# Kernel optimization log

Measured on AMD Instinct MI355X. Metric: run time of the kernel, lower is better.

## Reference

```python
import jax, jax.numpy as jnp
import numpy as np

DEPTH = 24
DLAT = 80      # latent_dim
H = 8          # latent_heads
DH = 64        # latent_dim_head
INNER = H * DH # 512
FFD = 2 * DLAT # FeedForward mult=2 -> 160
B = 64         # hardcoded in forward reshape
N = 128        # hardcoded max_num_nodes
MHD = 20       # multi_hop_max_dist
EF = 3         # edge feature count (meaned over by edge encoder)
EPS = 1e-5


def _ln(x, g, b):
    m = x.mean(-1, keepdims=True)
    v = ((x - m) ** 2).mean(-1, keepdims=True)
    return (x - m) / jnp.sqrt(v + EPS) * g + b


def setup_inputs() -> dict:
    key = jax.random.key(0)
    ks = jax.random.split(key, 24)
    std = 0.02 / np.sqrt(DEPTH)
    inp = {}
    # integer graph inputs
    inp['spatial_pos'] = jax.random.randint(ks[0], (B, N, N), 0, 40, dtype=jnp.int32)
    inp['edge_input'] = jax.random.randint(ks[1], (B, N, N, MHD, EF), 0, 64, dtype=jnp.int32)
    inp['x_nodes'] = jax.random.randint(ks[2], (B, N), 0, 64, dtype=jnp.int32)
    inp['indeg'] = jax.random.randint(ks[3], (B, N), 0, 64, dtype=jnp.int32)
    inp['outdeg'] = jax.random.randint(ks[4], (B, N), 0, 64, dtype=jnp.int32)
    # embedding tables (init_params: Embedding std=0.02)
    inp['atom_emb'] = 0.02 * jax.random.normal(ks[5], (64, DLAT), dtype=jnp.float32)
    inp['indeg_emb'] = 0.02 * jax.random.normal(ks[6], (64, DLAT), dtype=jnp.float32)
    inp['outdeg_emb'] = 0.02 * jax.random.normal(ks[7], (64, DLAT), dtype=jnp.float32)
    inp['edge_emb'] = 0.02 * jax.random.normal(ks[8], (64, 1), dtype=jnp.float32)
    inp['edge_dis_w'] = 0.02 * jax.random.normal(ks[9], (40,), dtype=jnp.float32)
    inp['spatial_emb'] = 0.02 * jax.random.normal(ks[10], (40, 1), dtype=jnp.float32)
    # per-layer stacked params (init_params: Linear std=0.02/sqrt(depth), bias 0)
    inp['ln1_g'] = jnp.ones((DEPTH, DLAT), jnp.float32)
    inp['ln1_b'] = jnp.zeros((DEPTH, DLAT), jnp.float32)
    inp['Wq'] = std * jax.random.normal(ks[11], (DEPTH, DLAT, INNER), dtype=jnp.float32)
    inp['Wkv'] = std * jax.random.normal(ks[12], (DEPTH, DLAT, 2 * INNER), dtype=jnp.float32)
    inp['Wo'] = std * jax.random.normal(ks[13], (DEPTH, INNER, DLAT), dtype=jnp.float32)
    inp['bo'] = jnp.zeros((DEPTH, DLAT), jnp.float32)
    inp['ln2_g'] = jnp.ones((DEPTH, DLAT), jnp.float32)
    inp['ln2_b'] = jnp.zeros((DEPTH, DLAT), jnp.float32)
    inp['W1'] = std * jax.random.normal(ks[14], (DEPTH, DLAT, FFD), dtype=jnp.float32)
    inp['b1'] = jnp.zeros((DEPTH, FFD), jnp.float32)
    inp['W2'] = std * jax.random.normal(ks[15], (DEPTH, FFD, DLAT), dtype=jnp.float32)
    inp['b2'] = jnp.zeros((DEPTH, DLAT), jnp.float32)
    # final head: LayerNorm + Linear(latent_dim, 1)
    inp['lnf_g'] = jnp.ones((DLAT,), jnp.float32)
    inp['lnf_b'] = jnp.zeros((DLAT,), jnp.float32)
    inp['Wf'] = std * jax.random.normal(ks[16], (DLAT, 1), dtype=jnp.float32)
    inp['bf'] = jnp.zeros((1,), jnp.float32)
    return inp


def reference(spatial_pos, edge_input, x_nodes, indeg, outdeg,
              atom_emb, indeg_emb, outdeg_emb, edge_emb, edge_dis_w, spatial_emb,
              ln1_g, ln1_b, Wq, Wkv, Wo, bo, ln2_g, ln2_b, W1, b1, W2, b2,
              lnf_g, lnf_b, Wf, bf):
    # --- graph structural bias ---
    sp_bias = spatial_emb[spatial_pos, 0]                       # [B,N,N]
    sp = jnp.where(spatial_pos == 0, 1, spatial_pos)
    sp = jnp.where(sp > 1, sp - 1, sp)
    sp = jnp.clip(sp, 0, MHD)
    e = edge_emb[edge_input, 0].mean(axis=-1)                   # [B,N,N,MHD] (mean over edge feats)
    e = (e * edge_dis_w[:MHD]).sum(-1) / sp.astype(jnp.float32) # per-hop scale, sum hops, normalize
    bias = e + sp_bias                                          # [B,N,N]
    # --- node embeddings ---
    x = atom_emb[x_nodes] + indeg_emb[indeg] + outdeg_emb[outdeg]  # [B,N,DLAT]
    scale = DH ** -0.5

    def layer(x, p):
        g1, be1, wq, wkv, wo, bo_, g2, be2, w1, bb1, w2, bb2 = p
        h = _ln(x, g1, be1)
        q = (h @ wq).reshape(B, N, H, DH)
        kv = h @ wkv
        k = kv[..., :INNER].reshape(B, N, H, DH)
        v = kv[..., INNER:].reshape(B, N, H, DH)
        sim = jnp.einsum('bihd,bjhd->bhij', q, k) * scale + bias[:, None]
        a = jax.nn.softmax(sim, axis=-1)
        o = jnp.einsum('bhij,bjhd->bihd', a, v).reshape(B, N, INNER)
        x = o @ wo + bo_ + x
        h = _ln(x, g2, be2)
        x = jax.nn.gelu(h @ w1 + bb1, approximate=False) @ w2 + bb2 + x
        return x, None

    x, _ = jax.lax.scan(layer, x, (ln1_g, ln1_b, Wq, Wkv, Wo, bo, ln2_g, ln2_b, W1, b1, W2, b2))
    pooled = x.mean(axis=1)                                     # Reduce 'b n d -> b d'
    return _ln(pooled, lnf_g, lnf_b) @ Wf + bf                  # [B,1]
```

## Files before the change

kernel.cpp:

```cpp
#include <hip/hip_runtime.h>
#include <math.h>

#define BDIM 64
#define NNODE 128
#define DLAT 80
#define NHEAD 8
#define DH 64
#define INNER 512
#define FFD 160
#define DEPTH 24
#define MROWS (BDIM * NNODE)

using bf16x8 = __attribute__((ext_vector_type(8))) short;
using f32x4  = __attribute__((ext_vector_type(4))) float;

#define MFMA(a, b, c) __builtin_amdgcn_mfma_f32_16x16x32_bf16((a), (b), (c), 0, 0, 0)

static __device__ __forceinline__ short f2bf(float f) {
    union { float f; unsigned u; } v; v.f = f;
    unsigned r = v.u + 0x7fffu + ((v.u >> 16) & 1u);
    return (short)(r >> 16);
}

__global__ __launch_bounds__(256) void wconv_kernel(
    const float* __restrict__ in, short* __restrict__ out, int K, int N, int Kp)
{
    __shared__ float t[64][65];
    int L = blockIdx.z;
    const float* src = in + (size_t)L * K * N;
    short* dst = out + (size_t)L * N * Kp;
    int n0 = blockIdx.x * 64, k0 = blockIdx.y * 64;
    int tx = threadIdx.x & 63, ty = threadIdx.x >> 6;
    for (int ki = ty; ki < 64; ki += 4) {
        int k = k0 + ki, n = n0 + tx;
        t[ki][tx] = (k < K && n < N) ? src[(size_t)k * N + n] : 0.f;
    }
    __syncthreads();
    for (int ni = ty; ni < 64; ni += 4) {
        int n = n0 + ni, k = k0 + tx;
        if (n < N && k < Kp) dst[(size_t)n * Kp + k] = f2bf(t[tx][ni]);
    }
}

__global__ __launch_bounds__(256) void bias_kernel(
    const int* __restrict__ spp, const int* __restrict__ ei,
    const float* __restrict__ edge_emb, const float* __restrict__ edw,
    const float* __restrict__ sp_emb, float* __restrict__ biasb)
{
    __shared__ float ee[64], ew[20], se[40];
    int tid = threadIdx.x;
    if (tid < 64) ee[tid] = edge_emb[tid];
    if (tid < 20) ew[tid] = edw[tid];
    if (tid < 40) se[tid] = sp_emb[tid];
    __syncthreads();

    int idx = blockIdx.x * 256 + tid;
    int spv = spp[idx];
    float spb = se[spv];
    int sp = min(20, max(1, spv - 1));

    const int4* p = (const int4*)(ei + (size_t)idx * 60);
    int e[60];
#pragma unroll
    for (int t = 0; t < 15; ++t) {
        int4 v = p[t];
        e[4*t+0] = v.x; e[4*t+1] = v.y; e[4*t+2] = v.z; e[4*t+3] = v.w;
    }
    float acc = 0.f;
#pragma unroll
    for (int m = 0; m < 20; ++m) {
        float s = ee[e[3*m]] + ee[e[3*m+1]] + ee[e[3*m+2]];
        acc += s * ew[m];
    }
    biasb[idx] = acc * (1.0f/3.0f) / (float)sp + spb;
}

__global__ __launch_bounds__(256) void node_emb_kernel(
    const int* __restrict__ xn, const int* __restrict__ ind, const int* __restrict__ outd,
    const float* __restrict__ ae, const float* __restrict__ ie, const float* __restrict__ oe,
    float* __restrict__ x)
{
    int idx = blockIdx.x * 256 + threadIdx.x;
    int e = idx / DLAT, d = idx % DLAT;
    x[idx] = ae[xn[e]*DLAT + d] + ie[ind[e]*DLAT + d] + oe[outd[e]*DLAT + d];
}

__global__ __launch_bounds__(256) void ln1_kernel(
    const float* __restrict__ x, const float* __restrict__ g,
    const float* __restrict__ be, short* __restrict__ lnx)
{
    int row = blockIdx.x * 128 + (threadIdx.x >> 1), sub = threadIdx.x & 1;
    const float* xr = x + (size_t)row * DLAT + sub * 40;
    float4 v[10];
#pragma unroll
    for (int i = 0; i < 10; ++i) v[i] = *(const float4*)(xr + i * 4);
    float s = 0.f;
#pragma unroll
    for (int i = 0; i < 10; ++i) s += v[i].x + v[i].y + v[i].z + v[i].w;
    s += __shfl_xor(s, 1);
    float mean = s * 0.0125f;
    float var = 0.f;
#pragma unroll
    for (int i = 0; i < 10; ++i) {
        float d;
        d = v[i].x - mean; var += d * d;
        d = v[i].y - mean; var += d * d;
        d = v[i].z - mean; var += d * d;
        d = v[i].w - mean; var += d * d;
    }
    var += __shfl_xor(var, 1);
    float rstd = 1.0f / sqrtf(var * 0.0125f + 1e-5f);
    short* dst = lnx + (size_t)row * 96 + sub * 40;
#pragma unroll
    for (int i = 0; i < 10; ++i) {
        int c = sub * 40 + i * 4;
        float4 g4 = *(const float4*)(g + c);
        float4 b4 = *(const float4*)(be + c);
        short4 o;
        o.x = f2bf((v[i].x - mean) * rstd * g4.x + b4.x);
        o.y = f2bf((v[i].y - mean) * rstd * g4.y + b4.y);
        o.z = f2bf((v[i].z - mean) * rstd * g4.z + b4.z);
        o.w = f2bf((v[i].w - mean) * rstd * g4.w + b4.w);
        *(short4*)(dst + i * 4) = o;
    }
    short4 z4; z4.x = z4.y = z4.z = z4.w = 0;
    *(short4*)(lnx + (size_t)row * 96 + 80 + sub * 8) = z4;
    *(short4*)(lnx + (size_t)row * 96 + 84 + sub * 8) = z4;
}

__global__ __launch_bounds__(512, 4) void attn2_kernel(
    const short* __restrict__ lnx, const float* __restrict__ biasb,
    const short* __restrict__ Wq_t, const short* __restrict__ Wkv_t,
    short* __restrict__ obuf)
{
    extern __shared__ short smem[];
    short* qh  = smem;
    short* kh  = smem + 9216;
    short* vth = smem + 18432;
    short* ph  = smem;
    short* ot  = smem + 18432;

    int tid = threadIdx.x;
    int lane = tid & 63, w = tid >> 6, l15 = lane & 15, lk = lane >> 4;
    int b = blockIdx.x >> 3, h = blockIdx.x & 7;

    float breg[8][4];
    {
        const float* bp = biasb + ((size_t)b * NNODE + w * 16) * NNODE;
#pragma unroll
        for (int jf = 0; jf < 8; ++jf)
#pragma unroll
            for (int r = 0; r < 4; ++r)
                breg[jf][r] = bp[(lk * 4 + r) * NNODE + jf * 16 + l15];
    }

    {
        const short* lb = lnx + (size_t)b * NNODE * 96;
        bf16x8 a[3];
#pragma unroll
        for (int ss = 0; ss < 3; ++ss)
            a[ss] = *(const bf16x8*)(lb + (w * 16 + l15) * 96 + ss * 32 + lk * 8);

        {
            f32x4 acc[4] = {};
#pragma unroll
            for (int ss = 0; ss < 3; ++ss)
#pragma unroll
                for (int nf = 0; nf < 4; ++nf) {
                    bf16x8 bv = *(const bf16x8*)(Wq_t + (size_t)(h * 64 + nf * 16 + l15) * 96 + ss * 32 + lk * 8);
                    acc[nf] = MFMA(a[ss], bv, acc[nf]);
                }
#pragma unroll
            for (int nf = 0; nf < 4; ++nf)
#pragma unroll
                for (int r = 0; r < 4; ++r)
                    qh[(w * 16 + lk * 4 + r) * 72 + nf * 16 + l15] = f2bf(acc[nf][r]);
        }
        {
            f32x4 acc[4] = {};
#pragma unroll
            for (int ss = 0; ss < 3; ++ss)
#pragma unroll
                for (int nf = 0; nf < 4; ++nf) {
                    bf16x8 bv = *(const bf16x8*)(Wkv_t + (size_t)(h * 64 + nf * 16 + l15) * 96 + ss * 32 + lk * 8);
                    acc[nf] = MFMA(a[ss], bv, acc[nf]);
                }
#pragma unroll
            for (int nf = 0; nf < 4; ++nf)
#pragma unroll
                for (int r = 0; r < 4; ++r)
                    kh[(w * 16 + lk * 4 + r) * 72 + nf * 16 + l15] = f2bf(acc[nf][r]);
        }
        {
            f32x4 acc[4] = {};
#pragma unroll
            for (int ss = 0; ss < 3; ++ss)
#pragma unroll
                for (int nf = 0; nf < 4; ++nf) {
                    bf16x8 bv = *(const bf16x8*)(Wkv_t + (size_t)(INNER + h * 64 + nf * 16 + l15) * 96 + ss * 32 + lk * 8);
                    acc[nf] = MFMA(a[ss], bv, acc[nf]);
                }
#pragma unroll
            for (int nf = 0; nf < 4; ++nf)
#pragma unroll
                for (int r = 0; r < 4; ++r)
                    vth[(nf * 16 + l15) * 136 + w * 16 + lk * 4 + r] = f2bf(acc[nf][r]);
        }
    }
    __syncthreads();

    f32x4 sc[8] = {};
#pragma unroll
    for (int ss = 0; ss < 2; ++ss) {
        bf16x8 qa = *(const bf16x8*)(qh + (w * 16 + l15) * 72 + ss * 32 + lk * 8);
#pragma unroll
        for (int jf = 0; jf < 8; ++jf) {
            bf16x8 bv = *(const bf16x8*)(kh + (jf * 16 + l15) * 72 + ss * 32 + lk * 8);
            sc[jf] = MFMA(qa, bv, sc[jf]);
        }
    }
    __syncthreads();

    float rinv[4];
#pragma unroll
    for (int r = 0; r < 4; ++r) {
        float sv[8];
#pragma unroll
        for (int jf = 0; jf < 8; ++jf) sv[jf] = sc[jf][r] * 0.125f + breg[jf][r];
        float mx = sv[0];
#pragma unroll
        for (int jf = 1; jf < 8; ++jf) mx = fmaxf(mx, sv[jf]);
        mx = fmaxf(mx, __shfl_xor(mx, 1));
        mx = fmaxf(mx, __shfl_xor(mx, 2));
        mx = fmaxf(mx, __shfl_xor(mx, 4));
        mx = fmaxf(mx, __shfl_xor(mx, 8));
        float e[8], sum = 0.f;
#pragma unroll
        for (int jf = 0; jf < 8; ++jf) { e[jf] = __expf(sv[jf] - mx); sum += e[jf]; }
        sum += __shfl_xor(sum, 1);
        sum += __shfl_xor(sum, 2);
        sum += __shfl_xor(sum, 4);
        sum += __shfl_xor(sum, 8);
        rinv[r] = 1.0f / sum;
        int row = w * 16 + lk * 4 + r;
#pragma unroll
        for (int jf = 0; jf < 8; ++jf)
            ph[row * 136 + jf * 16 + l15] = f2bf(e[jf]);
    }
    __syncthreads();

    f32x4 o[4] = {};
#pragma unroll
    for (int ks = 0; ks < 4; ++ks) {
        bf16x8 pa = *(const bf16x8*)(ph + (w * 16 + l15) * 136 + ks * 32 + lk * 8);
#pragma unroll
        for (int nf = 0; nf < 4; ++nf) {
            bf16x8 bv = *(const bf16x8*)(vth + (nf * 16 + l15) * 136 + ks * 32 + lk * 8);
            o[nf] = MFMA(pa, bv, o[nf]);
        }
    }
    __syncthreads();

#pragma unroll
    for (int nf = 0; nf < 4; ++nf)
#pragma unroll
        for (int r = 0; r < 4; ++r)
            ot[(w * 16 + lk * 4 + r) * 68 + nf * 16 + l15] = f2bf(o[nf][r] * rinv[r]);
    __syncthreads();

    {
        int row = tid >> 2, q4 = tid & 3;
        const short* src = ot + row * 68 + q4 * 16;
        short* dst = obuf + ((size_t)b * NNODE + row) * INNER + h * 64 + q4 * 16;
#pragma unroll
        for (int qq = 0; qq < 4; ++qq)
            *(uint2*)(dst + qq * 4) = *(const uint2*)(src + qq * 4);
    }
}

__global__ __launch_bounds__(512, 2) void tail2_kernel(
    const short* __restrict__ obuf, const float* __restrict__ xin,
    const short* __restrict__ Wo_t, const float* __restrict__ boL,
    const float* __restrict__ g2, const float* __restrict__ be2,
    const short* __restrict__ W1_t, const float* __restrict__ b1L,
    const short* __restrict__ W2_t, const float* __restrict__ b2L,
    float* __restrict__ xout,
    const float* __restrict__ g1n, const float* __restrict__ be1n,
    short* __restrict__ lnx)
{
    __shared__ float xmid[32 * 84];
    __shared__ short h2s[32 * 104];
    __shared__ short ffhs[32 * 168];

    int tid = threadIdx.x;
    int lane = tid & 63, w = tid >> 6, l15 = lane & 15, lk = lane >> 4;
    int b = blockIdx.x >> 2, qq = blockIdx.x & 3;
    int R0 = qq * 32;
    int wr = w >> 2, wn = w & 3;

    int n0_5 = (wn == 0) ? 0 : (wn + 1);
    int nc_5 = (wn == 0) ? 2 : 1;
    int n0_10 = (wn < 2) ? wn * 3 : 6 + (wn - 2) * 2;
    int nc_10 = (wn < 2) ? 3 : 2;

    {
        const short* og = obuf + ((size_t)b * NNODE + R0) * INNER;
        f32x4 acc[2] = {};
#pragma unroll 4
        for (int ks = 0; ks < 16; ++ks) {
            bf16x8 aa = *(const bf16x8*)(og + (wr * 16 + l15) * INNER + lk * 8 + ks * 32);
#pragma unroll
            for (int j = 0; j < 2; ++j)
                if (j < nc_5) {
                    bf16x8 bv = *(const bf16x8*)(Wo_t + (size_t)((n0_5 + j) * 16 + l15) * INNER + lk * 8 + ks * 32);
                    acc[j] = MFMA(aa, bv, acc[j]);
                }
        }
#pragma unroll
        for (int j = 0; j < 2; ++j)
            if (j < nc_5)
#pragma unroll
                for (int r = 0; r < 4; ++r) {
                    int row = wr * 16 + lk * 4 + r, col = (n0_5 + j) * 16 + l15;
                    xmid[row * 84 + col] = acc[j][r] + boL[col] +
                        xin[((size_t)b * NNODE + R0 + row) * DLAT + col];
                }
    }
    __syncthreads();

    {
        int row = tid >> 4, sub = tid & 15;
        float v[5];
#pragma unroll
        for (int e = 0; e < 5; ++e) v[e] = xmid[row * 84 + sub * 5 + e];
        float s = v[0] + v[1] + v[2] + v[3] + v[4];
        s += __shfl_xor(s, 1); s += __shfl_xor(s, 2);
        s += __shfl_xor(s, 4); s += __shfl_xor(s, 8);
        float mean = s * 0.0125f;
        float var = 0.f;
#pragma unroll
        for (int e = 0; e < 5; ++e) { float d = v[e] - mean; var += d * d; }
        var += __shfl_xor(var, 1); var += __shfl_xor(var, 2);
        var += __shfl_xor(var, 4); var += __shfl_xor(var, 8);
        float rstd = 1.0f / sqrtf(var * 0.0125f + 1e-5f);
#pragma unroll
        for (int e = 0; e < 5; ++e) {
            int c = sub * 5 + e;
            h2s[row * 104 + c] = f2bf((v[e] - mean) * rstd * g2[c] + be2[c]);
        }
        if (sub < 4) {
            short4 z4; z4.x = z4.y = z4.z = z4.w = 0;
            *(short4*)(h2s + row * 104 + 80 + sub * 4) = z4;
        }
    }
    __syncthreads();

    {
        f32x4 acc[3] = {};
#pragma unroll
        for (int ss = 0; ss < 3; ++ss) {
            bf16x8 aa = *(const bf16x8*)(h2s + (wr * 16 + l15) * 104 + lk * 8 + ss * 32);
#pragma unroll
            for (int j = 0; j < 3; ++j)
                if (j < nc_10) {
                    bf16x8 bv = *(const bf16x8*)(W1_t + (size_t)((n0_10 + j) * 16 + l15) * 96 + lk * 8 + ss * 32);
                    acc[j] = MFMA(aa, bv, acc[j]);
                }
        }
#pragma unroll
        for (int j = 0; j < 3; ++j)
            if (j < nc_10)
#pragma unroll
                for (int r = 0; r < 4; ++r) {
                    int row = wr * 16 + lk * 4 + r, c = (n0_10 + j) * 16 + l15;
                    float vv = acc[j][r] + b1L[c];
                    vv = 0.5f * vv * (1.0f + erff(vv * 0.70710678118654752f));
                    ffhs[row * 168 + c] = f2bf(vv);
                }
    }
    __syncthreads();

    {
        f32x4 acc[2] = {};
#pragma unroll
        for (int ks = 0; ks < 5; ++ks) {
            bf16x8 aa = *(const bf16x8*)(ffhs + (wr * 16 + l15) * 168 + lk * 8 + ks * 32);
#pragma unroll
            for (int j = 0; j < 2; ++j)
                if (j < nc_5) {
                    bf16x8 bv = *(const bf16x8*)(W2_t + (size_t)((n0_5 + j) * 16 + l15) * FFD + lk * 8 + ks * 32);
                    acc[j] = MFMA(aa, bv, acc[j]);
                }
        }
#pragma unroll
        for (int j = 0; j < 2; ++j)
            if (j < nc_5)
#pragma unroll
                for (int r = 0; r < 4; ++r) {
                    int row = wr * 16 + lk * 4 + r, col = (n0_5 + j) * 16 + l15;
                    float vv = acc[j][r] + b2L[col] + xmid[row * 84 + col];
                    xout[((size_t)b * NNODE + R0 + row) * DLAT + col] = vv;
                    xmid[row * 84 + col] = vv;
                }
    }
    __syncthreads();

    if (g1n) {
        int row = tid >> 4, sub = tid & 15;
        float v[5];
#pragma unroll
        for (int e = 0; e < 5; ++e) v[e] = xmid[row * 84 + sub * 5 + e];
        float s = v[0] + v[1] + v[2] + v[3] + v[4];
        s += __shfl_xor(s, 1); s += __shfl_xor(s, 2);
        s += __shfl_xor(s, 4); s += __shfl_xor(s, 8);
        float mean = s * 0.0125f;
        float var = 0.f;
#pragma unroll
        for (int e = 0; e < 5; ++e) { float d = v[e] - mean; var += d * d; }
        var += __shfl_xor(var, 1); var += __shfl_xor(var, 2);
        var += __shfl_xor(var, 4); var += __shfl_xor(var, 8);
        float rstd = 1.0f / sqrtf(var * 0.0125f + 1e-5f);
        short* lr = lnx + ((size_t)b * NNODE + R0 + row) * 96;
#pragma unroll
        for (int e = 0; e < 5; ++e) {
            int c = sub * 5 + e;
            lr[c] = f2bf((v[e] - mean) * rstd * g1n[c] + be1n[c]);
        }
        if (sub < 8) { lr[80 + sub * 2] = 0; lr[81 + sub * 2] = 0; }
    }
}

__global__ __launch_bounds__(128) void final_kernel(
    const float* __restrict__ x, const float* __restrict__ g, const float* __restrict__ bta,
    const float* __restrict__ Wf, const float* __restrict__ bf, float* __restrict__ out)
{
    int bb = blockIdx.x;
    int t = threadIdx.x;
    __shared__ float pd[DLAT];
    __shared__ float red[2];
    __shared__ float rbuf[128];

    if (t < DLAT) {
        float s = 0.f;
        for (int n = 0; n < NNODE; ++n) s += x[((size_t)bb * NNODE + n) * DLAT + t];
        pd[t] = s * (1.0f / NNODE);
    }
    __syncthreads();
    if (t == 0) {
        float m = 0.f;
        for (int k = 0; k < DLAT; ++k) m += pd[k];
        m /= DLAT;
        float v = 0.f;
        for (int k = 0; k < DLAT; ++k) { float d = pd[k] - m; v += d * d; }
        v /= DLAT;
        red[0] = m; red[1] = 1.0f / sqrtf(v + 1e-5f);
    }
    __syncthreads();
    float contrib = 0.f;
    if (t < DLAT)
        contrib = ((pd[t] - red[0]) * red[1] * g[t] + bta[t]) * Wf[t];
    rbuf[t] = contrib;
    __syncthreads();
    if (t == 0) {
        float s = 0.f;
        for (int k = 0; k < DLAT; ++k) s += rbuf[k];
        out[bb] = s + bf[0];
    }
}

extern "C" void kernel_launch(void* const* d_in, const int* in_sizes, int n_in,
                              void* d_out, int out_size, void* d_ws, size_t ws_size,
                              hipStream_t stream)
{
    const int*   spatial_pos = (const int*)  d_in[0];
    const int*   edge_input  = (const int*)  d_in[1];
    const int*   x_nodes     = (const int*)  d_in[2];
    const int*   indeg       = (const int*)  d_in[3];
    const int*   outdeg      = (const int*)  d_in[4];
    const float* atom_emb    = (const float*)d_in[5];
    const float* indeg_emb   = (const float*)d_in[6];
    const float* outdeg_emb  = (const float*)d_in[7];
    const float* edge_emb    = (const float*)d_in[8];
    const float* edge_dis_w  = (const float*)d_in[9];
    const float* spatial_emb = (const float*)d_in[10];
    const float* ln1_g = (const float*)d_in[11];
    const float* ln1_b = (const float*)d_in[12];
    const float* Wq    = (const float*)d_in[13];
    const float* Wkv   = (const float*)d_in[14];
    const float* Wo    = (const float*)d_in[15];
    const float* bo    = (const float*)d_in[16];
    const float* ln2_g = (const float*)d_in[17];
    const float* ln2_b = (const float*)d_in[18];
    const float* W1    = (const float*)d_in[19];
    const float* b1    = (const float*)d_in[20];
    const float* W2    = (const float*)d_in[21];
    const float* b2    = (const float*)d_in[22];
    const float* lnf_g = (const float*)d_in[23];
    const float* lnf_b = (const float*)d_in[24];
    const float* Wf    = (const float*)d_in[25];
    const float* bf    = (const float*)d_in[26];

    char* wsb = (char*)d_ws;
    float* biasb = (float*)(wsb + 0);
    float* x0    = (float*)(wsb + 4194304);
    float* x1    = (float*)(wsb + 6815744);
    short* obuf  = (short*)(wsb + 9437184);
    short* Wq_t  = (short*)(wsb + 17825792);
    short* Wkv_t = (short*)(wsb + 20185088);
    short* Wo_t  = (short*)(wsb + 24903680);
    short* W1_t  = (short*)(wsb + 26869760);
    short* W2_t  = (short*)(wsb + 27607040);
    short* lnx   = (short*)(wsb + 28221440);

    static const int ATTN_LDS = 54272;
    hipFuncSetAttribute((const void*)attn2_kernel,
                        hipFuncAttributeMaxDynamicSharedMemorySize, ATTN_LDS);

    wconv_kernel<<<dim3(8, 2, 24), 256, 0, stream>>>(Wq,  Wq_t,  80, 512, 96);
    wconv_kernel<<<dim3(16, 2, 24), 256, 0, stream>>>(Wkv, Wkv_t, 80, 1024, 96);
    wconv_kernel<<<dim3(2, 8, 24), 256, 0, stream>>>(Wo,  Wo_t,  512, 80, 512);
    wconv_kernel<<<dim3(3, 2, 24), 256, 0, stream>>>(W1,  W1_t,  80, 160, 96);
    wconv_kernel<<<dim3(2, 3, 24), 256, 0, stream>>>(W2,  W2_t,  160, 80, 160);

    bias_kernel<<<4096, 256, 0, stream>>>(spatial_pos, edge_input, edge_emb,
                                          edge_dis_w, spatial_emb, biasb);
    node_emb_kernel<<<2560, 256, 0, stream>>>(x_nodes, indeg, outdeg,
                                              atom_emb, indeg_emb, outdeg_emb, x0);
    ln1_kernel<<<64, 256, 0, stream>>>(x0, ln1_g, ln1_b, lnx);

    for (int L = 0; L < DEPTH; ++L) {
        const float* xin  = (L & 1) ? x1 : x0;
        float*       xout = (L & 1) ? x0 : x1;
        attn2_kernel<<<512, 512, ATTN_LDS, stream>>>(
            lnx, biasb,
            Wq_t + (size_t)L * 512 * 96, Wkv_t + (size_t)L * 1024 * 96,
            obuf);
        const float* g1n  = (L < DEPTH - 1) ? (ln1_g + (L + 1) * DLAT) : nullptr;
        const float* be1n = (L < DEPTH - 1) ? (ln1_b + (L + 1) * DLAT) : nullptr;
        tail2_kernel<<<256, 512, 0, stream>>>(
            obuf, xin,
            Wo_t + (size_t)L * 80 * 512, bo + L * DLAT,
            ln2_g + L * DLAT, ln2_b + L * DLAT,
            W1_t + (size_t)L * 160 * 96, b1 + L * FFD,
            W2_t + (size_t)L * 80 * 160, b2 + L * DLAT,
            xout, g1n, be1n, lnx);
    }

    final_kernel<<<BDIM, 128, 0, stream>>>(x0, lnf_g, lnf_b, Wf, bf, (float*)d_out);
}
```

Measured before the change: 1.529 ms.

## Fuse whole forward into one persistent kernel with per-graph atomic flag sync

Replaces about fifty kernel launches (weight conversion, bias, embedding, LN, and per-layer attention and tail) with a single persistent kernel of 256 blocks. Each block owns one graph and 32 rows, keeps the residual stream in LDS, and syncs with the other three blocks of its graph through atomic counters instead of kernel boundaries. This removes launch gaps and global round trips of x between layers. In exchange each block now processes two heads serially, occupancy is limited by larger LDS use, and all 256 blocks must be co-resident or the spin-waits will deadlock.

```diff
diff --git a/kernel.cpp b/kernel.cpp
--- a/kernel.cpp
+++ b/kernel.cpp
@@ -4,12 +4,9 @@
 #define BDIM 64
 #define NNODE 128
 #define DLAT 80
-#define NHEAD 8
-#define DH 64
 #define INNER 512
 #define FFD 160
 #define DEPTH 24
-#define MROWS (BDIM * NNODE)
 
 using bf16x8 = __attribute__((ext_vector_type(8))) short;
 using f32x4  = __attribute__((ext_vector_type(4))) float;
@@ -22,127 +19,179 @@
     return (short)(r >> 16);
 }
 
-__global__ __launch_bounds__(256) void wconv_kernel(
-    const float* __restrict__ in, short* __restrict__ out, int K, int N, int Kp)
+__device__ __forceinline__ void wait_cnt(int* p, int target) {
+    if (threadIdx.x == 0)
+        while (__hip_atomic_load(p, __ATOMIC_ACQUIRE, __HIP_MEMORY_SCOPE_AGENT) < target)
+            __builtin_amdgcn_s_sleep(2);
+    __syncthreads();
+}
+__device__ __forceinline__ void arrive(int* p) {
+    __syncthreads();
+    if (threadIdx.x == 0)
+        __hip_atomic_fetch_add(p, 1, __ATOMIC_RELEASE, __HIP_MEMORY_SCOPE_AGENT);
+}
+
+__device__ __forceinline__ void conv_tile(
+    const float* __restrict__ src, short* __restrict__ dst,
+    int K, int N, int Kp, int n0, int k0, float* tbuf)
 {
-    __shared__ float t[64][65];
-    int L = blockIdx.z;
-    const float* src = in + (size_t)L * K * N;
-    short* dst = out + (size_t)L * N * Kp;
-    int n0 = blockIdx.x * 64, k0 = blockIdx.y * 64;
     int tx = threadIdx.x & 63, ty = threadIdx.x >> 6;
-    for (int ki = ty; ki < 64; ki += 4) {
+    for (int ki = ty; ki < 64; ki += 8) {
         int k = k0 + ki, n = n0 + tx;
-        t[ki][tx] = (k < K && n < N) ? src[(size_t)k * N + n] : 0.f;
+        tbuf[ki * 65 + tx] = (k < K && n < N) ? src[(size_t)k * N + n] : 0.f;
     }
     __syncthreads();
-    for (int ni = ty; ni < 64; ni += 4) {
+    for (int ni = ty; ni < 64; ni += 8) {
         int n = n0 + ni, k = k0 + tx;
-        if (n < N && k < Kp) dst[(size_t)n * Kp + k] = f2bf(t[tx][ni]);
-    }
-}
-
-__global__ __launch_bounds__(256) void bias_kernel(
+        if (n < N && k < Kp) dst[(size_t)n * Kp + k] = f2bf(tbuf[tx * 65 + ni]);
+    }
+    __syncthreads();
+}
+
+__device__ __forceinline__ void ln_rows_to_lnx(
+    const float* xper, int row, int sub,
+    const float* __restrict__ g, const float* __restrict__ be,
+    short* __restrict__ lnxbase)
+{
+    float v[5];
+#pragma unroll
+    for (int e = 0; e < 5; ++e) v[e] = xper[row * 84 + sub * 5 + e];
+    float s = v[0] + v[1] + v[2] + v[3] + v[4];
+    s += __shfl_xor(s, 1); s += __shfl_xor(s, 2);
+    s += __shfl_xor(s, 4); s += __shfl_xor(s, 8);
+    float mean = s * 0.0125f;
+    float var = 0.f;
+#pragma unroll
+    for (int e = 0; e < 5; ++e) { float d = v[e] - mean; var += d * d; }
+    var += __shfl_xor(var, 1); var += __shfl_xor(var, 2);
+    var += __shfl_xor(var, 4); var += __shfl_xor(var, 8);
+    float rstd = 1.0f / sqrtf(var * 0.0125f + 1e-5f);
+    short* lr = lnxbase + row * 96;
+#pragma unroll
+    for (int e = 0; e < 5; ++e) {
+        int c = sub * 5 + e;
+        lr[c] = f2bf((v[e] - mean) * rstd * g[c] + be[c]);
+    }
+    if (sub < 8) { lr[80 + sub * 2] = 0; lr[81 + sub * 2] = 0; }
+}
+
+__global__ __launch_bounds__(512, 2) void persist_kernel(
     const int* __restrict__ spp, const int* __restrict__ ei,
-    const float* __restrict__ edge_emb, const float* __restrict__ edw,
-    const float* __restrict__ sp_emb, float* __restrict__ biasb)
-{
-    __shared__ float ee[64], ew[20], se[40];
-    int tid = threadIdx.x;
-    if (tid < 64) ee[tid] = edge_emb[tid];
-    if (tid < 20) ew[tid] = edw[tid];
-    if (tid < 40) se[tid] = sp_emb[tid];
-    __syncthreads();
-
-    int idx = blockIdx.x * 256 + tid;
-    int spv = spp[idx];
-    float spb = se[spv];
-    int sp = min(20, max(1, spv - 1));
-
-    const int4* p = (const int4*)(ei + (size_t)idx * 60);
-    int e[60];
-#pragma unroll
-    for (int t = 0; t < 15; ++t) {
-        int4 v = p[t];
-        e[4*t+0] = v.x; e[4*t+1] = v.y; e[4*t+2] = v.z; e[4*t+3] = v.w;
-    }
-    float acc = 0.f;
-#pragma unroll
-    for (int m = 0; m < 20; ++m) {
-        float s = ee[e[3*m]] + ee[e[3*m+1]] + ee[e[3*m+2]];
-        acc += s * ew[m];
-    }
-    biasb[idx] = acc * (1.0f/3.0f) / (float)sp + spb;
-}
-
-__global__ __launch_bounds__(256) void node_emb_kernel(
     const int* __restrict__ xn, const int* __restrict__ ind, const int* __restrict__ outd,
     const float* __restrict__ ae, const float* __restrict__ ie, const float* __restrict__ oe,
-    float* __restrict__ x)
+    const float* __restrict__ edge_emb, const float* __restrict__ edw,
+    const float* __restrict__ sp_emb,
+    const float* __restrict__ Wq, const float* __restrict__ Wkv,
+    const float* __restrict__ Wo, const float* __restrict__ W1, const float* __restrict__ W2,
+    const float* __restrict__ ln1_g, const float* __restrict__ ln1_b,
+    const float* __restrict__ bo,
+    const float* __restrict__ ln2_g, const float* __restrict__ ln2_b,
+    const float* __restrict__ b1, const float* __restrict__ b2,
+    const float* __restrict__ lnf_g, const float* __restrict__ lnf_b,
+    const float* __restrict__ Wf, const float* __restrict__ bfp,
+    float* __restrict__ biasb, short* __restrict__ lnx, short* __restrict__ obuf,
+    float* __restrict__ xfin, float* __restrict__ outp,
+    short* __restrict__ Wq_t, short* __restrict__ Wkv_t, short* __restrict__ Wo_t,
+    short* __restrict__ W1_t, short* __restrict__ W2_t,
+    int* __restrict__ flags)
 {
-    int idx = blockIdx.x * 256 + threadIdx.x;
-    int e = idx / DLAT, d = idx % DLAT;
-    x[idx] = ae[xn[e]*DLAT + d] + ie[ind[e]*DLAT + d] + oe[outd[e]*DLAT + d];
-}
-
-__global__ __launch_bounds__(256) void ln1_kernel(
-    const float* __restrict__ x, const float* __restrict__ g,
-    const float* __restrict__ be, short* __restrict__ lnx)
-{
-    int row = blockIdx.x * 128 + (threadIdx.x >> 1), sub = threadIdx.x & 1;
-    const float* xr = x + (size_t)row * DLAT + sub * 40;
-    float4 v[10];
-#pragma unroll
-    for (int i = 0; i < 10; ++i) v[i] = *(const float4*)(xr + i * 4);
-    float s = 0.f;
-#pragma unroll
-    for (int i = 0; i < 10; ++i) s += v[i].x + v[i].y + v[i].z + v[i].w;
-    s += __shfl_xor(s, 1);
-    float mean = s * 0.0125f;
-    float var = 0.f;
-#pragma unroll
-    for (int i = 0; i < 10; ++i) {
-        float d;
-        d = v[i].x - mean; var += d * d;
-        d = v[i].y - mean; var += d * d;
-        d = v[i].z - mean; var += d * d;
-        d = v[i].w - mean; var += d * d;
-    }
-    var += __shfl_xor(var, 1);
-    float rstd = 1.0f / sqrtf(var * 0.0125f + 1e-5f);
-    short* dst = lnx + (size_t)row * 96 + sub * 40;
-#pragma unroll
-    for (int i = 0; i < 10; ++i) {
-        int c = sub * 40 + i * 4;
-        float4 g4 = *(const float4*)(g + c);
-        float4 b4 = *(const float4*)(be + c);
-        short4 o;
-        o.x = f2bf((v[i].x - mean) * rstd * g4.x + b4.x);
-        o.y = f2bf((v[i].y - mean) * rstd * g4.y + b4.y);
-        o.z = f2bf((v[i].z - mean) * rstd * g4.z + b4.z);
-        o.w = f2bf((v[i].w - mean) * rstd * g4.w + b4.w);
-        *(short4*)(dst + i * 4) = o;
-    }
-    short4 z4; z4.x = z4.y = z4.z = z4.w = 0;
-    *(short4*)(lnx + (size_t)row * 96 + 80 + sub * 8) = z4;
-    *(short4*)(lnx + (size_t)row * 96 + 84 + sub * 8) = z4;
-}
-
-__global__ __launch_bounds__(512, 4) void attn2_kernel(
-    const short* __restrict__ lnx, const float* __restrict__ biasb,
-    const short* __restrict__ Wq_t, const short* __restrict__ Wkv_t,
-    short* __restrict__ obuf)
-{
-    extern __shared__ short smem[];
-    short* qh  = smem;
-    short* kh  = smem + 9216;
-    short* vth = smem + 18432;
-    short* ph  = smem;
-    short* ot  = smem + 18432;
+    extern __shared__ char dyn[];
+    short* qh   = (short*)dyn;
+    short* kh   = (short*)(dyn + 18432);
+    short* vth  = (short*)(dyn + 36864);
+    short* ph   = (short*)dyn;
+    short* ot   = (short*)(dyn + 36864);
+    float* tbuf = (float*)dyn;
+    float* xper = (float*)(dyn + 54272);
+    short* h2s  = (short*)(dyn + 65024);
+    short* ffhs = (short*)(dyn + 71680);
+    float* fin  = (float*)(dyn + 82432);
 
     int tid = threadIdx.x;
     int lane = tid & 63, w = tid >> 6, l15 = lane & 15, lk = lane >> 4;
-    int b = blockIdx.x >> 3, h = blockIdx.x & 7;
+    int bid = blockIdx.x;
+    int b = bid >> 2, g = bid & 3;
+    int R0 = g * 32;
+
+    int* ca = flags + b * DEPTH;
+    int* ct = flags + 1536 + b * (DEPTH + 1);
+    int* wflag = flags + 3136;
+
+#pragma unroll 1
+    for (int t = bid; t < 1824; t += 256) {
+        if (t < 384) {
+            int L = t >> 4, r = t & 15;
+            conv_tile(Wq + (size_t)L * 80 * 512, Wq_t + (size_t)L * 512 * 96,
+                      80, 512, 96, (r >> 1) * 64, (r & 1) * 64, tbuf);
+        } else if (t < 1152) {
+            int u = t - 384; int L = u >> 5, r = u & 31;
+            conv_tile(Wkv + (size_t)L * 80 * 1024, Wkv_t + (size_t)L * 1024 * 96,
+                      80, 1024, 96, (r >> 1) * 64, (r & 1) * 64, tbuf);
+        } else if (t < 1536) {
+            int u = t - 1152; int L = u >> 4, r = u & 15;
+            conv_tile(Wo + (size_t)L * 512 * 80, Wo_t + (size_t)L * 80 * 512,
+                      512, 80, 512, (r & 1) * 64, (r >> 1) * 64, tbuf);
+        } else if (t < 1680) {
+            int u = t - 1536; int L = u / 6, r = u % 6;
+            conv_tile(W1 + (size_t)L * 80 * 160, W1_t + (size_t)L * 160 * 96,
+                      80, 160, 96, (r % 3) * 64, (r / 3) * 64, tbuf);
+        } else {
+            int u = t - 1680; int L = u / 6, r = u % 6;
+            conv_tile(W2 + (size_t)L * 160 * 80, W2_t + (size_t)L * 80 * 160,
+                      160, 80, 160, (r & 1) * 64, (r / 2) * 64, tbuf);
+        }
+    }
+    if (tid == 0)
+        __hip_atomic_fetch_add(wflag, 1, __ATOMIC_RELEASE, __HIP_MEMORY_SCOPE_AGENT);
+
+    {
+        float* ee = (float*)h2s;
+        float* ew = ee + 64;
+        float* se = ee + 84;
+        if (tid < 64) ee[tid] = edge_emb[tid];
+        else if (tid < 84) ew[tid - 64] = edw[tid - 64];
+        else if (tid < 124) se[tid - 84] = sp_emb[tid - 84];
+        __syncthreads();
+        size_t base = ((size_t)b * NNODE + R0) * NNODE + (size_t)tid * 8;
+#pragma unroll 1
+        for (int u = 0; u < 8; ++u) {
+            size_t idx = base + u;
+            int spv = spp[idx];
+            float spb = se[spv];
+            int sp = min(20, max(1, spv - 1));
+            const int4* p = (const int4*)(ei + idx * 60);
+            int e[60];
+#pragma unroll
+            for (int t4 = 0; t4 < 15; ++t4) {
+                int4 v = p[t4];
+                e[4*t4+0] = v.x; e[4*t4+1] = v.y; e[4*t4+2] = v.z; e[4*t4+3] = v.w;
+            }
+            float acc = 0.f;
+#pragma unroll
+            for (int m = 0; m < 20; ++m) {
+                float s3 = ee[e[3*m]] + ee[e[3*m+1]] + ee[e[3*m+2]];
+                acc += s3 * ew[m];
+            }
+            biasb[idx] = acc * (1.0f/3.0f) / (float)sp + spb;
+        }
+        __syncthreads();
+    }
+
+    {
+        int row = tid >> 4, sub = tid & 15;
+        int node = b * NNODE + R0 + row;
+        int xv = xn[node] * DLAT, iv = ind[node] * DLAT, ov = outd[node] * DLAT;
+#pragma unroll
+        for (int e = 0; e < 5; ++e) {
+            int c = sub * 5 + e;
+            xper[row * 84 + c] = ae[xv + c] + ie[iv + c] + oe[ov + c];
+        }
+        __syncthreads();
+        ln_rows_to_lnx(xper, row, sub, ln1_g, ln1_b, lnx + ((size_t)b * NNODE + R0) * 96);
+    }
+    arrive(ct + 0);
+    wait_cnt(ct + 0, 4);
+    wait_cnt(wflag, 256);
 
     float breg[8][4];
     {
@@ -154,317 +203,294 @@
                 breg[jf][r] = bp[(lk * 4 + r) * NNODE + jf * 16 + l15];
     }
 
-    {
-        const short* lb = lnx + (size_t)b * NNODE * 96;
-        bf16x8 a[3];
-#pragma unroll
-        for (int ss = 0; ss < 3; ++ss)
-            a[ss] = *(const bf16x8*)(lb + (w * 16 + l15) * 96 + ss * 32 + lk * 8);
-
+#pragma unroll 1
+    for (int L = 0; L < DEPTH; ++L) {
+        const short* WqL  = Wq_t  + (size_t)L * INNER * 96;
+        const short* WkvL = Wkv_t + (size_t)L * 1024 * 96;
+        const short* WoL  = Wo_t  + (size_t)L * DLAT * INNER;
+        const short* W1L  = W1_t  + (size_t)L * FFD * 96;
+        const short* W2L  = W2_t  + (size_t)L * DLAT * FFD;
+        const float* boL  = bo + L * DLAT;
+        const float* g2L  = ln2_g + L * DLAT;
+        const float* be2L = ln2_b + L * DLAT;
+        const float* b1L  = b1 + L * FFD;
+        const float* b2L  = b2 + L * DLAT;
+
+        if (L > 0) wait_cnt(ct + L, 4);
+        bf16x8 av0, av1, av2;
         {
-            f32x4 acc[4] = {};
-#pragma unroll
-            for (int ss = 0; ss < 3; ++ss)
-#pragma unroll
-                for (int nf = 0; nf < 4; ++nf) {
-                    bf16x8 bv = *(const bf16x8*)(Wq_t + (size_t)(h * 64 + nf * 16 + l15) * 96 + ss * 32 + lk * 8);
-                    acc[nf] = MFMA(a[ss], bv, acc[nf]);
-                }
+            const short* lb = lnx + (size_t)b * NNODE * 96 + (w * 16 + l15) * 96 + lk * 8;
+            av0 = *(const bf16x8*)(lb);
+            av1 = *(const bf16x8*)(lb + 32);
+            av2 = *(const bf16x8*)(lb + 64);
+        }
+        bf16x8 av[3] = {av0, av1, av2};
+#pragma unroll 1
+        for (int hh = 0; hh < 2; ++hh) {
+            int h = g * 2 + hh;
+            if (hh) __syncthreads();
+            {
+                f32x4 acc[4] = {};
+#pragma unroll
+                for (int ss = 0; ss < 3; ++ss) {
+                    const short* wp = WqL + (size_t)(h * 64 + l15) * 96 + ss * 32 + lk * 8;
+#pragma unroll
+                    for (int nf = 0; nf < 4; ++nf)
+                        acc[nf] = MFMA(av[ss], *(const bf16x8*)(wp + nf * 16 * 96), acc[nf]);
+                }
+#pragma unroll
+                for (int nf = 0; nf < 4; ++nf)
+#pragma unroll
+                    for (int r = 0; r < 4; ++r)
+                        qh[(w * 16 + lk * 4 + r) * 72 + nf * 16 + l15] = f2bf(acc[nf][r]);
+            }
+            {
+                f32x4 acc[4] = {};
+#pragma unroll
+                for (int ss = 0; ss < 3; ++ss) {
+                    const short* wp = WkvL + (size_t)(h * 64 + l15) * 96 + ss * 32 + lk * 8;
+#pragma unroll
+                    for (int nf = 0; nf < 4; ++nf)
+                        acc[nf] = MFMA(av[ss], *(const bf16x8*)(wp + nf * 16 * 96), acc[nf]);
+                }
+#pragma unroll
+                for (int nf = 0; nf < 4; ++nf)
+#pragma unroll
+                    for (int r = 0; r < 4; ++r)
+                        kh[(w * 16 + lk * 4 + r) * 72 + nf * 16 + l15] = f2bf(acc[nf][r]);
+            }
+            {
+                f32x4 acc[4] = {};
+#pragma unroll
+                for (int ss = 0; ss < 3; ++ss) {
+                    const short* wp = WkvL + (size_t)(INNER + h * 64 + l15) * 96 + ss * 32 + lk * 8;
+#pragma unroll
+                    for (int nf = 0; nf < 4; ++nf)
+                        acc[nf] = MFMA(av[ss], *(const bf16x8*)(wp + nf * 16 * 96), acc[nf]);
+                }
+#pragma unroll
+                for (int nf = 0; nf < 4; ++nf)
+#pragma unroll
+                    for (int r = 0; r < 4; ++r)
+                        vth[(nf * 16 + l15) * 136 + w * 16 + lk * 4 + r] = f2bf(acc[nf][r]);
+            }
+            __syncthreads();
+
+            f32x4 sc[8] = {};
+#pragma unroll
+            for (int ss = 0; ss < 2; ++ss) {
+                bf16x8 qa = *(const bf16x8*)(qh + (w * 16 + l15) * 72 + ss * 32 + lk * 8);
+#pragma unroll
+                for (int jf = 0; jf < 8; ++jf)
+                    sc[jf] = MFMA(qa, *(const bf16x8*)(kh + (jf * 16 + l15) * 72 + ss * 32 + lk * 8), sc[jf]);
+            }
+            __syncthreads();
+
+            float rinv[4];
+#pragma unroll
+            for (int r = 0; r < 4; ++r) {
+                float sv[8];
+#pragma unroll
+                for (int jf = 0; jf < 8; ++jf) sv[jf] = sc[jf][r] * 0.125f + breg[jf][r];
+                float mx = sv[0];
+#pragma unroll
+                for (int jf = 1; jf < 8; ++jf) mx = fmaxf(mx, sv[jf]);
+                mx = fmaxf(mx, __shfl_xor(mx, 1));
+                mx = fmaxf(mx, __shfl_xor(mx, 2));
+                mx = fmaxf(mx, __shfl_xor(mx, 4));
+                mx = fmaxf(mx, __shfl_xor(mx, 8));
+                float e[8], sum = 0.f;
+#pragma unroll
+                for (int jf = 0; jf < 8; ++jf) { e[jf] = __expf(sv[jf] - mx); sum += e[jf]; }
+                sum += __shfl_xor(sum, 1);
+                sum += __shfl_xor(sum, 2);
+                sum += __shfl_xor(sum, 4);
+                sum += __shfl_xor(sum, 8);
+                rinv[r] = 1.0f / sum;
+                int row = w * 16 + lk * 4 + r;
+#pragma unroll
+                for (int jf = 0; jf < 8; ++jf)
+                    ph[row * 136 + jf * 16 + l15] = f2bf(e[jf]);
+            }
+            __syncthreads();
+
+            f32x4 o[4] = {};
+#pragma unroll
+            for (int ks = 0; ks < 4; ++ks) {
+                bf16x8 pa = *(const bf16x8*)(ph + (w * 16 + l15) * 136 + ks * 32 + lk * 8);
+#pragma unroll
+                for (int nf = 0; nf < 4; ++nf)
+                    o[nf] = MFMA(pa, *(const bf16x8*)(vth + (nf * 16 + l15) * 136 + ks * 32 + lk * 8), o[nf]);
+            }
+            __syncthreads();
+
 #pragma unroll
             for (int nf = 0; nf < 4; ++nf)
 #pragma unroll
                 for (int r = 0; r < 4; ++r)
-                    qh[(w * 16 + lk * 4 + r) * 72 + nf * 16 + l15] = f2bf(acc[nf][r]);
-        }
+                    ot[(w * 16 + lk * 4 + r) * 68 + nf * 16 + l15] = f2bf(o[nf][r] * rinv[r]);
+            __syncthreads();
+
+            {
+                int row = tid >> 2, q4 = tid & 3;
+                const short* src = ot + row * 68 + q4 * 16;
+                short* dst = obuf + ((size_t)b * NNODE + row) * INNER + h * 64 + q4 * 16;
+#pragma unroll
+                for (int qq = 0; qq < 4; ++qq)
+                    *(uint2*)(dst + qq * 4) = *(const uint2*)(src + qq * 4);
+            }
+        }
+        arrive(ca + L);
+
+        wait_cnt(ca + L, 4);
         {
-            f32x4 acc[4] = {};
-#pragma unroll
-            for (int ss = 0; ss < 3; ++ss)
-#pragma unroll
-                for (int nf = 0; nf < 4; ++nf) {
-                    bf16x8 bv = *(const bf16x8*)(Wkv_t + (size_t)(h * 64 + nf * 16 + l15) * 96 + ss * 32 + lk * 8);
-                    acc[nf] = MFMA(a[ss], bv, acc[nf]);
-                }
-#pragma unroll
-            for (int nf = 0; nf < 4; ++nf)
-#pragma unroll
-                for (int r = 0; r < 4; ++r)
-                    kh[(w * 16 + lk * 4 + r) * 72 + nf * 16 + l15] = f2bf(acc[nf][r]);
-        }
-        {
-            f32x4 acc[4] = {};
-#pragma unroll
-            for (int ss = 0; ss < 3; ++ss)
-#pragma unroll
-                for (int nf = 0; nf < 4; ++nf) {
-                    bf16x8 bv = *(const bf16x8*)(Wkv_t + (size_t)(INNER + h * 64 + nf * 16 + l15) * 96 + ss * 32 + lk * 8);
-                    acc[nf] = MFMA(a[ss], bv, acc[nf]);
-                }
-#pragma unroll
-            for (int nf = 0; nf < 4; ++nf)
-#pragma unroll
-                for (int r = 0; r < 4; ++r)
-                    vth[(nf * 16 + l15) * 136 + w * 16 + lk * 4 + r] = f2bf(acc[nf][r]);
-        }
-    }
-    __syncthreads();
-
-    f32x4 sc[8] = {};
-#pragma unroll
-    for (int ss = 0; ss < 2; ++ss) {
-        bf16x8 qa = *(const bf16x8*)(qh + (w * 16 + l15) * 72 + ss * 32 + lk * 8);
-#pragma unroll
-        for (int jf = 0; jf < 8; ++jf) {
-            bf16x8 bv = *(const bf16x8*)(kh + (jf * 16 + l15) * 72 + ss * 32 + lk * 8);
-            sc[jf] = MFMA(qa, bv, sc[jf]);
-        }
-    }
-    __syncthreads();
-
-    float rinv[4];
-#pragma unroll
-    for (int r = 0; r < 4; ++r) {
-        float sv[8];
-#pragma unroll
-        for (int jf = 0; jf < 8; ++jf) sv[jf] = sc[jf][r] * 0.125f + breg[jf][r];
-        float mx = sv[0];
-#pragma unroll
-        for (int jf = 1; jf < 8; ++jf) mx = fmaxf(mx, sv[jf]);
-        mx = fmaxf(mx, __shfl_xor(mx, 1));
-        mx = fmaxf(mx, __shfl_xor(mx, 2));
-        mx = fmaxf(mx, __shfl_xor(mx, 4));
-        mx = fmaxf(mx, __shfl_xor(mx, 8));
-        float e[8], sum = 0.f;
-#pragma unroll
-        for (int jf = 0; jf < 8; ++jf) { e[jf] = __expf(sv[jf] - mx); sum += e[jf]; }
-        sum += __shfl_xor(sum, 1);
-        sum += __shfl_xor(sum, 2);
-        sum += __shfl_xor(sum, 4);
-        sum += __shfl_xor(sum, 8);
-        rinv[r] = 1.0f / sum;
-        int row = w * 16 + lk * 4 + r;
-#pragma unroll
-        for (int jf = 0; jf < 8; ++jf)
-            ph[row * 136 + jf * 16 + l15] = f2bf(e[jf]);
-    }
-    __syncthreads();
-
-    f32x4 o[4] = {};
-#pragma unroll
-    for (int ks = 0; ks < 4; ++ks) {
-        bf16x8 pa = *(const bf16x8*)(ph + (w * 16 + l15) * 136 + ks * 32 + lk * 8);
-#pragma unroll
-        for (int nf = 0; nf < 4; ++nf) {
-            bf16x8 bv = *(const bf16x8*)(vth + (nf * 16 + l15) * 136 + ks * 32 + lk * 8);
-            o[nf] = MFMA(pa, bv, o[nf]);
-        }
-    }
-    __syncthreads();
-
-#pragma unroll
-    for (int nf = 0; nf < 4; ++nf)
-#pragma unroll
-        for (int r = 0; r < 4; ++r)
-            ot[(w * 16 + lk * 4 + r) * 68 + nf * 16 + l15] = f2bf(o[nf][r] * rinv[r]);
-    __syncthreads();
-
-    {
-        int row = tid >> 2, q4 = tid & 3;
-        const short* src = ot + row * 68 + q4 * 16;
-        short* dst = obuf + ((size_t)b * NNODE + row) * INNER + h * 64 + q4 * 16;
-#pragma unroll
-        for (int qq = 0; qq < 4; ++qq)
-            *(uint2*)(dst + qq * 4) = *(const uint2*)(src + qq * 4);
-    }
-}
-
-__global__ __launch_bounds__(512, 2) void tail2_kernel(
-    const short* __restrict__ obuf, const float* __restrict__ xin,
-    const short* __restrict__ Wo_t, const float* __restrict__ boL,
-    const float* __restrict__ g2, const float* __restrict__ be2,
-    const short* __restrict__ W1_t, const float* __restrict__ b1L,
-    const short* __restrict__ W2_t, const float* __restrict__ b2L,
-    float* __restrict__ xout,
-    const float* __restrict__ g1n, const float* __restrict__ be1n,
-    short* __restrict__ lnx)
-{
-    __shared__ float xmid[32 * 84];
-    __shared__ short h2s[32 * 104];
-    __shared__ short ffhs[32 * 168];
-
-    int tid = threadIdx.x;
-    int lane = tid & 63, w = tid >> 6, l15 = lane & 15, lk = lane >> 4;
-    int b = blockIdx.x >> 2, qq = blockIdx.x & 3;
-    int R0 = qq * 32;
-    int wr = w >> 2, wn = w & 3;
-
-    int n0_5 = (wn == 0) ? 0 : (wn + 1);
-    int nc_5 = (wn == 0) ? 2 : 1;
-    int n0_10 = (wn < 2) ? wn * 3 : 6 + (wn - 2) * 2;
-    int nc_10 = (wn < 2) ? 3 : 2;
-
-    {
-        const short* og = obuf + ((size_t)b * NNODE + R0) * INNER;
-        f32x4 acc[2] = {};
+            int wr = w >> 2, wn = w & 3;
+            int n0_5 = (wn == 0) ? 0 : (wn + 1), nc_5 = (wn == 0) ? 2 : 1;
+            int n0_10 = (wn < 2) ? wn * 3 : 6 + (wn - 2) * 2, nc_10 = (wn < 2) ? 3 : 2;
+
+            {
+                const short* og = obuf + ((size_t)b * NNODE + R0) * INNER;
+                f32x4 acc[2] = {};
 #pragma unroll 4
-        for (int ks = 0; ks < 16; ++ks) {
-            bf16x8 aa = *(const bf16x8*)(og + (wr * 16 + l15) * INNER + lk * 8 + ks * 32);
-#pragma unroll
-            for (int j = 0; j < 2; ++j)
-                if (j < nc_5) {
-                    bf16x8 bv = *(const bf16x8*)(Wo_t + (size_t)((n0_5 + j) * 16 + l15) * INNER + lk * 8 + ks * 32);
-                    acc[j] = MFMA(aa, bv, acc[j]);
-                }
-        }
-#pragma unroll
-        for (int j = 0; j < 2; ++j)
-            if (j < nc_5)
-#pragma unroll
-                for (int r = 0; r < 4; ++r) {
-                    int row = wr * 16 + lk * 4 + r, col = (n0_5 + j) * 16 + l15;
-                    xmid[row * 84 + col] = acc[j][r] + boL[col] +
-                        xin[((size_t)b * NNODE + R0 + row) * DLAT + col];
-                }
-    }
-    __syncthreads();
-
-    {
-        int row = tid >> 4, sub = tid & 15;
-        float v[5];
-#pragma unroll
-        for (int e = 0; e < 5; ++e) v[e] = xmid[row * 84 + sub * 5 + e];
-        float s = v[0] + v[1] + v[2] + v[3] + v[4];
-        s += __shfl_xor(s, 1); s += __shfl_xor(s, 2);
-        s += __shfl_xor(s, 4); s += __shfl_xor(s, 8);
-        float mean = s * 0.0125f;
-        float var = 0.f;
-#pragma unroll
-        for (int e = 0; e < 5; ++e) { float d = v[e] - mean; var += d * d; }
-        var += __shfl_xor(var, 1); var += __shfl_xor(var, 2);
-        var += __shfl_xor(var, 4); var += __shfl_xor(var, 8);
-        float rstd = 1.0f / sqrtf(var * 0.0125f + 1e-5f);
-#pragma unroll
-        for (int e = 0; e < 5; ++e) {
-            int c = sub * 5 + e;
-            h2s[row * 104 + c] = f2bf((v[e] - mean) * rstd * g2[c] + be2[c]);
-        }
-        if (sub < 4) {
-            short4 z4; z4.x = z4.y = z4.z = z4.w = 0;
-            *(short4*)(h2s + row * 104 + 80 + sub * 4) = z4;
-        }
-    }
-    __syncthreads();
-
-    {
-        f32x4 acc[3] = {};
-#pragma unroll
-        for (int ss = 0; ss < 3; ++ss) {
-            bf16x8 aa = *(const bf16x8*)(h2s + (wr * 16 + l15) * 104 + lk * 8 + ss * 32);
-#pragma unroll
-            for (int j = 0; j < 3; ++j)
-                if (j < nc_10) {
-                    bf16x8 bv = *(const bf16x8*)(W1_t + (size_t)((n0_10 + j) * 16 + l15) * 96 + lk * 8 + ss * 32);
-                    acc[j] = MFMA(aa, bv, acc[j]);
-                }
-        }
-#pragma unroll
-        for (int j = 0; j < 3; ++j)
-            if (j < nc_10)
-#pragma unroll
-                for (int r = 0; r < 4; ++r) {
-                    int row = wr * 16 + lk * 4 + r, c = (n0_10 + j) * 16 + l15;
-                    float vv = acc[j][r] + b1L[c];
-                    vv = 0.5f * vv * (1.0f + erff(vv * 0.70710678118654752f));
-                    ffhs[row * 168 + c] = f2bf(vv);
-                }
-    }
-    __syncthreads();
-
-    {
-        f32x4 acc[2] = {};
-#pragma unroll
-        for (int ks = 0; ks < 5; ++ks) {
-            bf16x8 aa = *(const bf16x8*)(ffhs + (wr * 16 + l15) * 168 + lk * 8 + ks * 32);
-#pragma unroll
-            for (int j = 0; j < 2; ++j)
-                if (j < nc_5) {
-                    bf16x8 bv = *(const bf16x8*)(W2_t + (size_t)((n0_5 + j) * 16 + l15) * FFD + lk * 8 + ks * 32);
-                    acc[j] = MFMA(aa, bv, acc[j]);
-                }
-        }
-#pragma unroll
-        for (int j = 0; j < 2; ++j)
-            if (j < nc_5)
-#pragma unroll
-                for (int r = 0; r < 4; ++r) {
-                    int row = wr * 16 + lk * 4 + r, col = (n0_5 + j) * 16 + l15;
-                    float vv = acc[j][r] + b2L[col] + xmid[row * 84 + col];
-                    xout[((size_t)b * NNODE + R0 + row) * DLAT + col] = vv;
-                    xmid[row * 84 + col] = vv;
-                }
-    }
-    __syncthreads();
-
-    if (g1n) {
-        int row = tid >> 4, sub = tid & 15;
-        float v[5];
-#pragma unroll
-        for (int e = 0; e < 5; ++e) v[e] = xmid[row * 84 + sub * 5 + e];
-        float s = v[0] + v[1] + v[2] + v[3] + v[4];
-        s += __shfl_xor(s, 1); s += __shfl_xor(s, 2);
-        s += __shfl_xor(s, 4); s += __shfl_xor(s, 8);
-        float mean = s * 0.0125f;
-        float var = 0.f;
-#pragma unroll
-        for (int e = 0; e < 5; ++e) { float d = v[e] - mean; var += d * d; }
-        var += __shfl_xor(var, 1); var += __shfl_xor(var, 2);
-        var += __shfl_xor(var, 4); var += __shfl_xor(var, 8);
-        float rstd = 1.0f / sqrtf(var * 0.0125f + 1e-5f);
-        short* lr = lnx + ((size_t)b * NNODE + R0 + row) * 96;
-#pragma unroll
-        for (int e = 0; e < 5; ++e) {
-            int c = sub * 5 + e;
-            lr[c] = f2bf((v[e] - mean) * rstd * g1n[c] + be1n[c]);
-        }
-        if (sub < 8) { lr[80 + sub * 2] = 0; lr[81 + sub * 2] = 0; }
-    }
-}
-
-__global__ __launch_bounds__(128) void final_kernel(
-    const float* __restrict__ x, const float* __restrict__ g, const float* __restrict__ bta,
-    const float* __restrict__ Wf, const float* __restrict__ bf, float* __restrict__ out)
-{
-    int bb = blockIdx.x;
-    int t = threadIdx.x;
-    __shared__ float pd[DLAT];
-    __shared__ float red[2];
-    __shared__ float rbuf[128];
-
-    if (t < DLAT) {
-        float s = 0.f;
-        for (int n = 0; n < NNODE; ++n) s += x[((size_t)bb * NNODE + n) * DLAT + t];
-        pd[t] = s * (1.0f / NNODE);
-    }
-    __syncthreads();
-    if (t == 0) {
-        float m = 0.f;
-        for (int k = 0; k < DLAT; ++k) m += pd[k];
-        m /= DLAT;
-        float v = 0.f;
-        for (int k = 0; k < DLAT; ++k) { float d = pd[k] - m; v += d * d; }
-        v /= DLAT;
-        red[0] = m; red[1] = 1.0f / sqrtf(v + 1e-5f);
-    }
-    __syncthreads();
-    float contrib = 0.f;
-    if (t < DLAT)
-        contrib = ((pd[t] - red[0]) * red[1] * g[t] + bta[t]) * Wf[t];
-    rbuf[t] = contrib;
-    __syncthreads();
-    if (t == 0) {
-        float s = 0.f;
-        for (int k = 0; k < DLAT; ++k) s += rbuf[k];
-        out[bb] = s + bf[0];
+                for (int ks = 0; ks < 16; ++ks) {
+                    bf16x8 aa = *(const bf16x8*)(og + (wr * 16 + l15) * INNER + lk * 8 + ks * 32);
+#pragma unroll
+                    for (int j = 0; j < 2; ++j)
+                        if (j < nc_5) {
+                            bf16x8 bv = *(const bf16x8*)(WoL + (size_t)((n0_5 + j) * 16 + l15) * INNER + lk * 8 + ks * 32);
+                            acc[j] = MFMA(aa, bv, acc[j]);
+                        }
+                }
+#pragma unroll
+                for (int j = 0; j < 2; ++j)
+                    if (j < nc_5)
+#pragma unroll
+                        for (int r = 0; r < 4; ++r) {
+                            int row = wr * 16 + lk * 4 + r, col = (n0_5 + j) * 16 + l15;
+                            xper[row * 84 + col] += acc[j][r] + boL[col];
+                        }
+            }
+            __syncthreads();
+
+            {
+                int row = tid >> 4, sub = tid & 15;
+                float v[5];
+#pragma unroll
+                for (int e = 0; e < 5; ++e) v[e] = xper[row * 84 + sub * 5 + e];
+                float s = v[0] + v[1] + v[2] + v[3] + v[4];
+                s += __shfl_xor(s, 1); s += __shfl_xor(s, 2);
+                s += __shfl_xor(s, 4); s += __shfl_xor(s, 8);
+                float mean = s * 0.0125f;
+                float var = 0.f;
+#pragma unroll
+                for (int e = 0; e < 5; ++e) { float d = v[e] - mean; var += d * d; }
+                var += __shfl_xor(var, 1); var += __shfl_xor(var, 2);
+                var += __shfl_xor(var, 4); var += __shfl_xor(var, 8);
+                float rstd = 1.0f / sqrtf(var * 0.0125f + 1e-5f);
+#pragma unroll
+                for (int e = 0; e < 5; ++e) {
+                    int c = sub * 5 + e;
+                    h2s[row * 104 + c] = f2bf((v[e] - mean) * rstd * g2L[c] + be2L[c]);
+                }
+                if (sub < 4) {
+                    short4 z4; z4.x = z4.y = z4.z = z4.w = 0;
+                    *(short4*)(h2s + row * 104 + 80 + sub * 4) = z4;
+                }
+            }
+            __syncthreads();
+
+            {
+                f32x4 acc[3] = {};
+#pragma unroll
+                for (int ss = 0; ss < 3; ++ss) {
+                    bf16x8 aa = *(const bf16x8*)(h2s + (wr * 16 + l15) * 104 + lk * 8 + ss * 32);
+#pragma unroll
+                    for (int j = 0; j < 3; ++j)
+                        if (j < nc_10) {
+                            bf16x8 bv = *(const bf16x8*)(W1L + (size_t)((n0_10 + j) * 16 + l15) * 96 + lk * 8 + ss * 32);
+                            acc[j] = MFMA(aa, bv, acc[j]);
+                        }
+                }
+#pragma unroll
+                for (int j = 0; j < 3; ++j)
+                    if (j < nc_10)
+#pragma unroll
+                        for (int r = 0; r < 4; ++r) {
+                            int row = wr * 16 + lk * 4 + r, c = (n0_10 + j) * 16 + l15;
+                            float vv = acc[j][r] + b1L[c];
+                            vv = 0.5f * vv * (1.0f + erff(vv * 0.70710678118654752f));
+                            ffhs[row * 168 + c] = f2bf(vv);
+                        }
+            }
+            __syncthreads();
+
+            {
+                f32x4 acc[2] = {};
+#pragma unroll
+                for (int ks = 0; ks < 5; ++ks) {
+                    bf16x8 aa = *(const bf16x8*)(ffhs + (wr * 16 + l15) * 168 + lk * 8 + ks * 32);
+#pragma unroll
+                    for (int j = 0; j < 2; ++j)
+                        if (j < nc_5) {
+                            bf16x8 bv = *(const bf16x8*)(W2L + (size_t)((n0_5 + j) * 16 + l15) * FFD + lk * 8 + ks * 32);
+                            acc[j] = MFMA(aa, bv, acc[j]);
+                        }
+                }
+#pragma unroll
+                for (int j = 0; j < 2; ++j)
+                    if (j < nc_5)
+#pragma unroll
+                        for (int r = 0; r < 4; ++r) {
+                            int row = wr * 16 + lk * 4 + r, col = (n0_5 + j) * 16 + l15;
+                            float vv = acc[j][r] + b2L[col] + xper[row * 84 + col];
+                            xper[row * 84 + col] = vv;
+                            if (L == DEPTH - 1)
+                                xfin[((size_t)b * NNODE + R0 + row) * DLAT + col] = vv;
+                        }
+            }
+            __syncthreads();
+
+            if (L < DEPTH - 1) {
+                int row = tid >> 4, sub = tid & 15;
+                ln_rows_to_lnx(xper, row, sub,
+                               ln1_g + (L + 1) * DLAT, ln1_b + (L + 1) * DLAT,
+                               lnx + ((size_t)b * NNODE + R0) * 96);
+            }
+        }
+        arrive(ct + L + 1);
+    }
+
+    if (g == 0) {
+        wait_cnt(ct + DEPTH, 4);
+        float* pd = fin;
+        float* red = fin + 80;
+        float* rb = fin + 82;
+        if (tid < DLAT) {
+            float s = 0.f;
+#pragma unroll 1
+            for (int n = 0; n < NNODE; ++n)
+                s += xfin[((size_t)b * NNODE + n) * DLAT + tid];
+            pd[tid] = s * (1.0f / NNODE);
+        }
+        __syncthreads();
+        if (tid == 0) {
+            float m = 0.f;
+            for (int k = 0; k < DLAT; ++k) m += pd[k];
+            m /= DLAT;
+            float v = 0.f;
+            for (int k = 0; k < DLAT; ++k) { float d = pd[k] - m; v += d * d; }
+            v /= DLAT;
+            red[0] = m; red[1] = 1.0f / sqrtf(v + 1e-5f);
+        }
+        __syncthreads();
+        if (tid < DLAT)
+            rb[tid] = ((pd[tid] - red[0]) * red[1] * lnf_g[tid] + lnf_b[tid]) * Wf[tid];
+        __syncthreads();
+        if (tid == 0) {
+            float s = 0.f;
+            for (int k = 0; k < DLAT; ++k) s += rb[k];
+            outp[b] = s + bfp[0];
+        }
     }
 }
 
@@ -502,8 +528,7 @@
 
     char* wsb = (char*)d_ws;
     float* biasb = (float*)(wsb + 0);
-    float* x0    = (float*)(wsb + 4194304);
-    float* x1    = (float*)(wsb + 6815744);
+    float* xfin  = (float*)(wsb + 4194304);
     short* obuf  = (short*)(wsb + 9437184);
     short* Wq_t  = (short*)(wsb + 17825792);
     short* Wkv_t = (short*)(wsb + 20185088);
@@ -511,40 +536,21 @@
     short* W1_t  = (short*)(wsb + 26869760);
     short* W2_t  = (short*)(wsb + 27607040);
     short* lnx   = (short*)(wsb + 28221440);
-
-    static const int ATTN_LDS = 54272;
-    hipFuncSetAttribute((const void*)attn2_kernel,
-                        hipFuncAttributeMaxDynamicSharedMemorySize, ATTN_LDS);
-
-    wconv_kernel<<<dim3(8, 2, 24), 256, 0, stream>>>(Wq,  Wq_t,  80, 512, 96);
-    wconv_kernel<<<dim3(16, 2, 24), 256, 0, stream>>>(Wkv, Wkv_t, 80, 1024, 96);
-    wconv_kernel<<<dim3(2, 8, 24), 256, 0, stream>>>(Wo,  Wo_t,  512, 80, 512);
-    wconv_kernel<<<dim3(3, 2, 24), 256, 0, stream>>>(W1,  W1_t,  80, 160, 96);
-    wconv_kernel<<<dim3(2, 3, 24), 256, 0, stream>>>(W2,  W2_t,  160, 80, 160);
-
-    bias_kernel<<<4096, 256, 0, stream>>>(spatial_pos, edge_input, edge_emb,
-                                          edge_dis_w, spatial_emb, biasb);
-    node_emb_kernel<<<2560, 256, 0, stream>>>(x_nodes, indeg, outdeg,
-                                              atom_emb, indeg_emb, outdeg_emb, x0);
-    ln1_kernel<<<64, 256, 0, stream>>>(x0, ln1_g, ln1_b, lnx);
-
-    for (int L = 0; L < DEPTH; ++L) {
-        const float* xin  = (L & 1) ? x1 : x0;
-        float*       xout = (L & 1) ? x0 : x1;
-        attn2_kernel<<<512, 512, ATTN_LDS, stream>>>(
-            lnx, biasb,
-            Wq_t + (size_t)L * 512 * 96, Wkv_t + (size_t)L * 1024 * 96,
-            obuf);
-        const float* g1n  = (L < DEPTH - 1) ? (ln1_g + (L + 1) * DLAT) : nullptr;
-        const float* be1n = (L < DEPTH - 1) ? (ln1_b + (L + 1) * DLAT) : nullptr;
-        tail2_kernel<<<256, 512, 0, stream>>>(
-            obuf, xin,
-            Wo_t + (size_t)L * 80 * 512, bo + L * DLAT,
-            ln2_g + L * DLAT, ln2_b + L * DLAT,
-            W1_t + (size_t)L * 160 * 96, b1 + L * FFD,
-            W2_t + (size_t)L * 80 * 160, b2 + L * DLAT,
-            xout, g1n, be1n, lnx);
-    }
-
-    final_kernel<<<BDIM, 128, 0, stream>>>(x0, lnf_g, lnf_b, Wf, bf, (float*)d_out);
-}
+    int*   flags = (int*)  (wsb + 29794304);
+
+    static const int LDSB = 83456;
+    hipFuncSetAttribute((const void*)persist_kernel,
+                        hipFuncAttributeMaxDynamicSharedMemorySize, LDSB);
+
+    hipMemsetAsync(flags, 0, 12548, stream);
+
+    persist_kernel<<<256, 512, LDSB, stream>>>(
+        spatial_pos, edge_input, x_nodes, indeg, outdeg,
+        atom_emb, indeg_emb, outdeg_emb, edge_emb, edge_dis_w, spatial_emb,
+        Wq, Wkv, Wo, W1, W2,
+        ln1_g, ln1_b, bo, ln2_g, ln2_b, b1, b2,
+        lnf_g, lnf_b, Wf, bf,
+        biasb, lnx, obuf, xfin, (float*)d_out,
+        Wq_t, Wkv_t, Wo_t, W1_t, W2_t,
+        flags);
+}
```

Measured after the change: 1.785 ms. 1.17x slower.
